# Performance work log

Measured on AMD Instinct MI355X. Metric: run time of the kernel, lower is better.

Reference implementation:

```python
import jax, jax.numpy as jnp
import numpy as np

EMBED_DIM = 1024
NUM_HEADS = 16
HEAD_DIM = EMBED_DIM // NUM_HEADS
BSZ = 8
SEQ = 1024


def setup_inputs() -> dict:
    key = jax.random.key(0)
    ks = jax.random.split(key, 8)
    s = 1.0 / np.sqrt(EMBED_DIM)
    return {
        "query": jax.random.normal(ks[0], (BSZ, SEQ, EMBED_DIM), jnp.float32),
        "key": jax.random.normal(ks[1], (BSZ, SEQ, EMBED_DIM), jnp.float32),
        "value": jax.random.normal(ks[2], (BSZ, SEQ, EMBED_DIM), jnp.float32),
        "Wq": jax.random.normal(ks[3], (EMBED_DIM, EMBED_DIM), jnp.float32) * s,
        "bq": jnp.zeros((EMBED_DIM,), jnp.float32),
        "Wk": jax.random.normal(ks[4], (EMBED_DIM, EMBED_DIM), jnp.float32) * s,
        "bk": jnp.zeros((EMBED_DIM,), jnp.float32),
        "Wv": jax.random.normal(ks[5], (EMBED_DIM, EMBED_DIM), jnp.float32) * s,
        "bv": jnp.zeros((EMBED_DIM,), jnp.float32),
        "Wo": jax.random.normal(ks[6], (EMBED_DIM, EMBED_DIM), jnp.float32) * s,
        "bo": jnp.zeros((EMBED_DIM,), jnp.float32),
    }


def reference(query, key, value, Wq, bq, Wk, bk, Wv, bv, Wo, bo):
    # B=0 path of hfta MultiheadAttention, dropout=0 (eval), no masks.
    bsz, tgt_len, embed_dim = query.shape
    src_len = key.shape[1]
    scaling = HEAD_DIM ** -0.5

    # torch Linear: y = x @ W.T + b
    q = (jnp.einsum('bte,fe->btf', query, Wq) + bq) * scaling
    k = jnp.einsum('bse,fe->bsf', key, Wk) + bk
    v = jnp.einsum('bse,fe->bsf', value, Wv) + bv

    # split heads: [b, h, t, d]
    q = q.reshape(bsz, tgt_len, NUM_HEADS, HEAD_DIM).transpose(0, 2, 1, 3)
    k = k.reshape(bsz, src_len, NUM_HEADS, HEAD_DIM).transpose(0, 2, 1, 3)
    v = v.reshape(bsz, src_len, NUM_HEADS, HEAD_DIM).transpose(0, 2, 1, 3)

    scores = jnp.einsum('bhtd,bhsd->bhts', q, k)          # [b,h,t,s]
    attn = jax.nn.softmax(scores, axis=-1)
    o = jnp.einsum('bhts,bhsd->bhtd', attn, v)            # [b,h,t,d]
    o = o.transpose(0, 2, 1, 3).reshape(bsz, tgt_len, embed_dim)
    o = jnp.einsum('bte,fe->btf', o, Wo) + bo
    return o
```

## Files before the change

### kernel.cpp

```cpp
#include <hip/hip_runtime.h>
#include <hip/hip_bf16.h>

#define BSZ   8
#define SEQ   1024
#define EMB   1024
#define NH    16
#define HD    64
#define MROWS (BSZ*SEQ)
#define LOG2E 1.44269504088896f

typedef short  short8  __attribute__((ext_vector_type(8)));
typedef short  short4v __attribute__((ext_vector_type(4)));
typedef float  floatx4 __attribute__((ext_vector_type(4)));
typedef unsigned int uint2v __attribute__((ext_vector_type(2)));
typedef unsigned int uint4v __attribute__((ext_vector_type(4)));

__device__ __forceinline__ unsigned short f2bf(float f) {
  union { float f; unsigned u; } v; v.f = f;
  unsigned r = v.u + 0x7FFFu + ((v.u >> 16) & 1u);
  return (unsigned short)(r >> 16);
}
__device__ __forceinline__ unsigned pk2bf(float a, float b) {
  __hip_bfloat162 t = __float22bfloat162_rn(make_float2(a, b));
  union { __hip_bfloat162 h; unsigned u; } c; c.h = t; return c.u;
}

__device__ __forceinline__ void g2lds16(const unsigned short* g, unsigned short* l) {
  __builtin_amdgcn_global_load_lds(
      (const __attribute__((address_space(1))) unsigned int*)g,
      (__attribute__((address_space(3))) unsigned int*)l, 16, 0, 0);
}

__global__ __launch_bounds__(256) void convert_w4(
    const float* __restrict__ w0, const float* __restrict__ w1,
    const float* __restrict__ w2, const float* __restrict__ w3,
    unsigned short* __restrict__ out, float qs)
{
  const int z = blockIdx.y;
  const float* w = (z == 0) ? w0 : (z == 1) ? w1 : (z == 2) ? w2 : w3;
  const float s = (z == 0) ? qs : 1.0f;
  int i = blockIdx.x * 256 + threadIdx.x;
  float4 f = ((const float4*)w)[i];
  short4v p;
  p.x = (short)f2bf(f.x * s); p.y = (short)f2bf(f.y * s);
  p.z = (short)f2bf(f.z * s); p.w = (short)f2bf(f.w * s);
  ((short4v*)(out + (size_t)z * EMB * EMB))[i] = p;
}

template<int QKV>
__global__ __launch_bounds__(256) void gemm_k(
    const float* __restrict__ A0, const float* __restrict__ A1,
    const float* __restrict__ A2,
    const unsigned short* __restrict__ Abf,
    const unsigned short* __restrict__ Wbase,
    const float* __restrict__ b0, const float* __restrict__ b1,
    const float* __restrict__ b2, float qs,
    unsigned short* __restrict__ obf, float* __restrict__ of32)
{
  __shared__ __align__(16) unsigned short As[128 * 64];
  __shared__ __align__(16) unsigned short Ws[128 * 64];
  const int tid  = threadIdx.x;
  const int lane = tid & 63, wid = tid >> 6;
  const int z    = QKV ? blockIdx.z : 0;
  const int n0   = blockIdx.x * 128;
  const int m0   = blockIdx.y * 128;
  const int wm = (wid & 1) * 64, wn = (wid >> 1) * 64;
  const int quad = lane >> 4, ln = lane & 15, e3 = ln & 7;
  const int lrow = lane >> 3;
  const int lcol8 = ((lane & 7) ^ lrow) * 8;

  const unsigned short* W = Wbase + (size_t)z * EMB * EMB;
  const float* Af = QKV ? ((z == 0) ? A0 : (z == 1) ? A1 : A2) : (const float*)0;
  const int ar = tid >> 1;
  const int ac = (tid & 1) * 32;

  floatx4 acc[4][4] = {};

  for (int k0 = 0; k0 < EMB; k0 += 64) {
    if (QKV) {
      const float* src = Af + (size_t)(m0 + ar) * EMB + k0 + ac;
#pragma unroll
      for (int i = 0; i < 4; i++) {
        float4 x = *(const float4*)(src + i * 8);
        float4 y = *(const float4*)(src + i * 8 + 4);
        uint4v u;
        u.x = pk2bf(x.x, x.y); u.y = pk2bf(x.z, x.w);
        u.z = pk2bf(y.x, y.y); u.w = pk2bf(y.z, y.w);
        int ch = (4 * (tid & 1) + i) ^ (ar & 7);
        *(uint4v*)&As[ar * 64 + ch * 8] = u;
      }
#pragma unroll
      for (int c = 0; c < 4; c++) {
        int r = wid * 32 + c * 8;
        g2lds16(W + (size_t)(n0 + r + lrow) * EMB + k0 + lcol8, &Ws[r * 64]);
      }
    } else {
#pragma unroll
      for (int c = 0; c < 4; c++) {
        int r = wid * 32 + c * 8;
        g2lds16(Abf + (size_t)(m0 + r + lrow) * EMB + k0 + lcol8, &As[r * 64]);
        g2lds16(W   + (size_t)(n0 + r + lrow) * EMB + k0 + lcol8, &Ws[r * 64]);
      }
    }
    __syncthreads();
#pragma unroll
    for (int ks = 0; ks < 2; ks++) {
      short8 af[4], wf[4];
#pragma unroll
      for (int t = 0; t < 4; t++) {
        int pc = ((4 * ks + quad) ^ e3) * 8;
        af[t] = *(const short8*)&As[(wm + t * 16 + ln) * 64 + pc];
        wf[t] = *(const short8*)&Ws[(wn + t * 16 + ln) * 64 + pc];
      }
#pragma unroll
      for (int mi = 0; mi < 4; mi++)
#pragma unroll
        for (int ni = 0; ni < 4; ni++)
          acc[mi][ni] = __builtin_amdgcn_mfma_f32_16x16x32_bf16(
              af[mi], wf[ni], acc[mi][ni], 0, 0, 0);
    }
    __syncthreads();
  }

  const float* bias = QKV ? ((z == 0) ? b0 : (z == 1) ? b1 : b2) : b0;
  const float bsc = (QKV && z == 0) ? qs : 1.0f;
  unsigned short* outz = obf + (size_t)z * MROWS * EMB;

#pragma unroll
  for (int mi = 0; mi < 4; mi++) {
#pragma unroll
    for (int ni = 0; ni < 4; ni++) {
      int gn = n0 + wn + ni * 16 + ln;
      float bv = bsc * bias[gn];
      int gmb = m0 + wm + mi * 16 + quad * 4;
      if (!QKV) {
#pragma unroll
        for (int r = 0; r < 4; r++)
          of32[(size_t)(gmb + r) * EMB + gn] = acc[mi][ni][r] + bv;
      } else if (z < 2) {
        int h = gn >> 6, d = gn & 63;
#pragma unroll
        for (int r = 0; r < 4; r++) {
          int gm = gmb + r;
          int b = gm >> 10, s = gm & 1023;
          outz[((size_t)(b * NH + h) * SEQ + s) * HD + d] = f2bf(acc[mi][ni][r] + bv);
        }
      } else {
        int h = gn >> 6, d = gn & 63;
        int b = gmb >> 10, s = gmb & 1023;
        short4v pkt;
        pkt.x = (short)f2bf(acc[mi][ni][0] + bv);
        pkt.y = (short)f2bf(acc[mi][ni][1] + bv);
        pkt.z = (short)f2bf(acc[mi][ni][2] + bv);
        pkt.w = (short)f2bf(acc[mi][ni][3] + bv);
        *(short4v*)&outz[((size_t)(b * NH + h) * HD + d) * SEQ + s] = pkt;
      }
    }
  }
}

__global__ __launch_bounds__(256) void attn_k(
    const unsigned short* __restrict__ q,
    const unsigned short* __restrict__ k,
    const unsigned short* __restrict__ vt,
    unsigned short* __restrict__ o)
{
  __shared__ __align__(16) unsigned short Ks[64 * 64];
  __shared__ __align__(16) unsigned short Vs[64 * 64];
  __shared__ __align__(16) unsigned short Pb[4][16][72];
  const int tid  = threadIdx.x;
  const int lane = tid & 63, wv = tid >> 6;
  const int quad = lane >> 4, ln = lane & 15, e3 = ln & 7;
  const int bh = blockIdx.x >> 4;
  const int t0 = (blockIdx.x & 15) * 64 + wv * 16;
  const int b = bh >> 4, h = bh & 15;
  const int lrow = lane >> 3;
  const int lcol8 = ((lane & 7) ^ lrow) * 8;

  const unsigned short* qh = q  + (size_t)bh * SEQ * HD;
  const unsigned short* kh = k  + (size_t)bh * SEQ * HD;
  const unsigned short* vh = vt + (size_t)bh * HD * SEQ;

  short8 qf[2];
#pragma unroll
  for (int kc = 0; kc < 2; kc++)
    qf[kc] = *(const short8*)(qh + (size_t)(t0 + ln) * HD + kc * 32 + quad * 8);

  const short ONE = (short)0x3F80;
  const short8 onesf = {ONE, ONE, ONE, ONE, ONE, ONE, ONE, ONE};

  floatx4 Oa[4] = {};
  floatx4 Ol  = {};

  for (int s0 = 0; s0 < SEQ; s0 += 64) {
#pragma unroll
    for (int c = 0; c < 2; c++) {
      int ch = wv * 2 + c;
      g2lds16(kh + (size_t)(s0 + ch * 8 + lrow) * HD + lcol8,  &Ks[ch * 8 * 64]);
      g2lds16(vh + (size_t)(ch * 8 + lrow) * SEQ + s0 + lcol8, &Vs[ch * 8 * 64]);
    }
    __syncthreads();

    floatx4 sc[4];
#pragma unroll
    for (int st = 0; st < 4; st++) {
      floatx4 a = {};
      short8 kf0 = *(const short8*)&Ks[(st * 16 + ln) * 64 + ((0 + quad) ^ e3) * 8];
      short8 kf1 = *(const short8*)&Ks[(st * 16 + ln) * 64 + ((4 + quad) ^ e3) * 8];
      a = __builtin_amdgcn_mfma_f32_16x16x32_bf16(kf0, qf[0], a, 0, 0, 0);
      a = __builtin_amdgcn_mfma_f32_16x16x32_bf16(kf1, qf[1], a, 0, 0, 0);
      sc[st] = a;
    }

#pragma unroll
    for (int st = 0; st < 4; st++) {
      uint2v u;
      u.x = pk2bf(exp2f(sc[st][0]), exp2f(sc[st][1]));
      u.y = pk2bf(exp2f(sc[st][2]), exp2f(sc[st][3]));
      *(uint2v*)&Pb[wv][ln][st * 16 + quad * 4] = u;
    }

#pragma unroll
    for (int kc = 0; kc < 2; kc++) {
      short8 pf = *(const short8*)&Pb[wv][ln][kc * 32 + quad * 8];
#pragma unroll
      for (int di = 0; di < 4; di++) {
        short8 vf = *(const short8*)&Vs[(di * 16 + ln) * 64 + ((4 * kc + quad) ^ e3) * 8];
        Oa[di] = __builtin_amdgcn_mfma_f32_16x16x32_bf16(vf, pf, Oa[di], 0, 0, 0);
      }
      Ol = __builtin_amdgcn_mfma_f32_16x16x32_bf16(onesf, pf, Ol, 0, 0, 0);
    }
    __syncthreads();
  }

  float linv = 1.0f / Ol[0];
  size_t rowbase = (size_t)(b * SEQ + t0 + ln) * EMB + h * HD;
#pragma unroll
  for (int di = 0; di < 4; di++) {
    uint2v pkt;
    pkt.x = pk2bf(Oa[di][0] * linv, Oa[di][1] * linv);
    pkt.y = pk2bf(Oa[di][2] * linv, Oa[di][3] * linv);
    *(uint2v*)&o[rowbase + di * 16 + quad * 4] = pkt;
  }
}

extern "C" void kernel_launch(void* const* d_in, const int* in_sizes, int n_in,
                              void* d_out, int out_size, void* d_ws, size_t ws_size,
                              hipStream_t stream) {
  const float* query = (const float*)d_in[0];
  const float* key   = (const float*)d_in[1];
  const float* value = (const float*)d_in[2];
  const float* Wq = (const float*)d_in[3];
  const float* bq = (const float*)d_in[4];
  const float* Wk = (const float*)d_in[5];
  const float* bk = (const float*)d_in[6];
  const float* Wv = (const float*)d_in[7];
  const float* bv = (const float*)d_in[8];
  const float* Wo = (const float*)d_in[9];
  const float* bo = (const float*)d_in[10];
  float* out = (float*)d_out;

  unsigned short* ws = (unsigned short*)d_ws;
  const size_t WSZ = (size_t)EMB * EMB;
  const size_t TSZ = (size_t)MROWS * EMB;
  unsigned short* Wb   = ws;
  unsigned short* q_b  = Wb + 4 * WSZ;
  unsigned short* k_b  = q_b + TSZ;
  unsigned short* vt_b = k_b + TSZ;
  unsigned short* o_b  = vt_b + TSZ;

  const float qscale = 0.125f * LOG2E;

  convert_w4<<<dim3((int)(WSZ / 4 / 256), 4), 256, 0, stream>>>(Wq, Wk, Wv, Wo, Wb, qscale);

  gemm_k<1><<<dim3(EMB / 128, MROWS / 128, 3), 256, 0, stream>>>(
      query, key, value, (const unsigned short*)0, Wb,
      bq, bk, bv, qscale, q_b, (float*)0);

  attn_k<<<dim3(BSZ * NH * (SEQ / 64)), 256, 0, stream>>>(q_b, k_b, vt_b, o_b);

  gemm_k<0><<<dim3(EMB / 128, MROWS / 128, 1), 256, 0, stream>>>(
      (const float*)0, (const float*)0, (const float*)0, o_b, Wb + 3 * WSZ,
      bo, (const float*)0, (const float*)0, 1.0f, (unsigned short*)0, out);
}
```

Baseline: 385.3 us.

## Double-buffer GEMM and attention LDS tiles; process four query tiles per attention block

```diff
diff --git a/kernel.cpp b/kernel.cpp
--- a/kernel.cpp
+++ b/kernel.cpp
@@ -48,7 +48,7 @@
 }
 
 template<int QKV>
-__global__ __launch_bounds__(256) void gemm_k(
+__global__ __launch_bounds__(256, 2) void gemm_k(
     const float* __restrict__ A0, const float* __restrict__ A1,
     const float* __restrict__ A2,
     const unsigned short* __restrict__ Abf,
@@ -57,8 +57,8 @@
     const float* __restrict__ b2, float qs,
     unsigned short* __restrict__ obf, float* __restrict__ of32)
 {
-  __shared__ __align__(16) unsigned short As[128 * 64];
-  __shared__ __align__(16) unsigned short Ws[128 * 64];
+  __shared__ __align__(16) unsigned short As[2][128 * 64];
+  __shared__ __align__(16) unsigned short Ws[2][128 * 64];
   const int tid  = threadIdx.x;
   const int lane = tid & 63, wid = tid >> 6;
   const int z    = QKV ? blockIdx.z : 0;
@@ -75,42 +75,56 @@
   const int ac = (tid & 1) * 32;
 
   floatx4 acc[4][4] = {};
-
-  for (int k0 = 0; k0 < EMB; k0 += 64) {
-    if (QKV) {
-      const float* src = Af + (size_t)(m0 + ar) * EMB + k0 + ac;
-#pragma unroll
-      for (int i = 0; i < 4; i++) {
-        float4 x = *(const float4*)(src + i * 8);
-        float4 y = *(const float4*)(src + i * 8 + 4);
-        uint4v u;
-        u.x = pk2bf(x.x, x.y); u.y = pk2bf(x.z, x.w);
-        u.z = pk2bf(y.x, y.y); u.w = pk2bf(y.z, y.w);
-        int ch = (4 * (tid & 1) + i) ^ (ar & 7);
-        *(uint4v*)&As[ar * 64 + ch * 8] = u;
+  float4 ax[8];
+
+  if (QKV) {
+    const float* src = Af + (size_t)(m0 + ar) * EMB + ac;
+#pragma unroll
+    for (int i = 0; i < 8; i++) ax[i] = *(const float4*)(src + i * 4);
+  }
+#pragma unroll
+  for (int c = 0; c < 4; c++) {
+    int r = wid * 32 + c * 8;
+    g2lds16(W + (size_t)(n0 + r + lrow) * EMB + lcol8, &Ws[0][r * 64]);
+    if (!QKV) g2lds16(Abf + (size_t)(m0 + r + lrow) * EMB + lcol8, &As[0][r * 64]);
+  }
+  if (QKV) {
+#pragma unroll
+    for (int i = 0; i < 4; i++) {
+      uint4v u;
+      u.x = pk2bf(ax[2*i].x, ax[2*i].y);     u.y = pk2bf(ax[2*i].z, ax[2*i].w);
+      u.z = pk2bf(ax[2*i+1].x, ax[2*i+1].y); u.w = pk2bf(ax[2*i+1].z, ax[2*i+1].w);
+      int ch = (4 * (tid & 1) + i) ^ (ar & 7);
+      *(uint4v*)&As[0][ar * 64 + ch * 8] = u;
+    }
+  }
+
+  const int NK = EMB / 64;
+  for (int it = 0; it < NK; ++it) {
+    __syncthreads();
+    const int cb = it & 1, nb = (it + 1) & 1;
+    if (it < NK - 1) {
+      const int k1 = (it + 1) * 64;
+      if (QKV) {
+        const float* src = Af + (size_t)(m0 + ar) * EMB + k1 + ac;
+#pragma unroll
+        for (int i = 0; i < 8; i++) ax[i] = *(const float4*)(src + i * 4);
       }
 #pragma unroll
       for (int c = 0; c < 4; c++) {
         int r = wid * 32 + c * 8;
-        g2lds16(W + (size_t)(n0 + r + lrow) * EMB + k0 + lcol8, &Ws[r * 64]);
-      }
-    } else {
-#pragma unroll
-      for (int c = 0; c < 4; c++) {
-        int r = wid * 32 + c * 8;
-        g2lds16(Abf + (size_t)(m0 + r + lrow) * EMB + k0 + lcol8, &As[r * 64]);
-        g2lds16(W   + (size_t)(n0 + r + lrow) * EMB + k0 + lcol8, &Ws[r * 64]);
-      }
-    }
-    __syncthreads();
+        g2lds16(W + (size_t)(n0 + r + lrow) * EMB + k1 + lcol8, &Ws[nb][r * 64]);
+        if (!QKV) g2lds16(Abf + (size_t)(m0 + r + lrow) * EMB + k1 + lcol8, &As[nb][r * 64]);
+      }
+    }
 #pragma unroll
     for (int ks = 0; ks < 2; ks++) {
       short8 af[4], wf[4];
 #pragma unroll
       for (int t = 0; t < 4; t++) {
         int pc = ((4 * ks + quad) ^ e3) * 8;
-        af[t] = *(const short8*)&As[(wm + t * 16 + ln) * 64 + pc];
-        wf[t] = *(const short8*)&Ws[(wn + t * 16 + ln) * 64 + pc];
+        af[t] = *(const short8*)&As[cb][(wm + t * 16 + ln) * 64 + pc];
+        wf[t] = *(const short8*)&Ws[cb][(wn + t * 16 + ln) * 64 + pc];
       }
 #pragma unroll
       for (int mi = 0; mi < 4; mi++)
@@ -119,7 +133,16 @@
           acc[mi][ni] = __builtin_amdgcn_mfma_f32_16x16x32_bf16(
               af[mi], wf[ni], acc[mi][ni], 0, 0, 0);
     }
-    __syncthreads();
+    if (QKV && it < NK - 1) {
+#pragma unroll
+      for (int i = 0; i < 4; i++) {
+        uint4v u;
+        u.x = pk2bf(ax[2*i].x, ax[2*i].y);     u.y = pk2bf(ax[2*i].z, ax[2*i].w);
+        u.z = pk2bf(ax[2*i+1].x, ax[2*i+1].y); u.w = pk2bf(ax[2*i+1].z, ax[2*i+1].w);
+        int ch = (4 * (tid & 1) + i) ^ (ar & 7);
+        *(uint4v*)&As[nb][ar * 64 + ch * 8] = u;
+      }
+    }
   }
 
   const float* bias = QKV ? ((z == 0) ? b0 : (z == 1) ? b1 : b2) : b0;
@@ -159,20 +182,20 @@
   }
 }
 
-__global__ __launch_bounds__(256) void attn_k(
+__global__ __launch_bounds__(256, 2) void attn_k(
     const unsigned short* __restrict__ q,
     const unsigned short* __restrict__ k,
     const unsigned short* __restrict__ vt,
     unsigned short* __restrict__ o)
 {
-  __shared__ __align__(16) unsigned short Ks[64 * 64];
-  __shared__ __align__(16) unsigned short Vs[64 * 64];
+  __shared__ __align__(16) unsigned short Ks[2][64 * 64];
+  __shared__ __align__(16) unsigned short Vs[2][64 * 64];
   __shared__ __align__(16) unsigned short Pb[4][16][72];
   const int tid  = threadIdx.x;
   const int lane = tid & 63, wv = tid >> 6;
   const int quad = lane >> 4, ln = lane & 15, e3 = ln & 7;
-  const int bh = blockIdx.x >> 4;
-  const int t0 = (blockIdx.x & 15) * 64 + wv * 16;
+  const int bh = blockIdx.x >> 2;
+  const int tb = (blockIdx.x & 3) * 256;
   const int b = bh >> 4, h = bh & 15;
   const int lrow = lane >> 3;
   const int lcol8 = ((lane & 7) ^ lrow) * 8;
@@ -181,66 +204,88 @@
   const unsigned short* kh = k  + (size_t)bh * SEQ * HD;
   const unsigned short* vh = vt + (size_t)bh * HD * SEQ;
 
-  short8 qf[2];
-#pragma unroll
-  for (int kc = 0; kc < 2; kc++)
-    qf[kc] = *(const short8*)(qh + (size_t)(t0 + ln) * HD + kc * 32 + quad * 8);
+  short8 qf[4][2];
+#pragma unroll
+  for (int tt = 0; tt < 4; tt++)
+#pragma unroll
+    for (int kc = 0; kc < 2; kc++)
+      qf[tt][kc] = *(const short8*)(qh +
+          (size_t)(tb + tt * 64 + wv * 16 + ln) * HD + kc * 32 + quad * 8);
 
   const short ONE = (short)0x3F80;
   const short8 onesf = {ONE, ONE, ONE, ONE, ONE, ONE, ONE, ONE};
 
-  floatx4 Oa[4] = {};
-  floatx4 Ol  = {};
-
-  for (int s0 = 0; s0 < SEQ; s0 += 64) {
-#pragma unroll
-    for (int c = 0; c < 2; c++) {
-      int ch = wv * 2 + c;
-      g2lds16(kh + (size_t)(s0 + ch * 8 + lrow) * HD + lcol8,  &Ks[ch * 8 * 64]);
-      g2lds16(vh + (size_t)(ch * 8 + lrow) * SEQ + s0 + lcol8, &Vs[ch * 8 * 64]);
-    }
+  floatx4 Oa[4][4] = {};
+  floatx4 Ol[4]    = {};
+
+#pragma unroll
+  for (int c = 0; c < 2; c++) {
+    int ch = wv * 2 + c;
+    g2lds16(kh + (size_t)(ch * 8 + lrow) * HD + lcol8,  &Ks[0][ch * 8 * 64]);
+    g2lds16(vh + (size_t)(ch * 8 + lrow) * SEQ + lcol8, &Vs[0][ch * 8 * 64]);
+  }
+
+  for (int it = 0; it < SEQ / 64; ++it) {
     __syncthreads();
-
-    floatx4 sc[4];
+    const int cb = it & 1, nb = (it + 1) & 1;
+    if (it < SEQ / 64 - 1) {
+      const int s1 = (it + 1) * 64;
+#pragma unroll
+      for (int c = 0; c < 2; c++) {
+        int ch = wv * 2 + c;
+        g2lds16(kh + (size_t)(s1 + ch * 8 + lrow) * HD + lcol8,  &Ks[nb][ch * 8 * 64]);
+        g2lds16(vh + (size_t)(ch * 8 + lrow) * SEQ + s1 + lcol8, &Vs[nb][ch * 8 * 64]);
+      }
+    }
+
+    short8 kf[4][2], vf[4][2];
 #pragma unroll
     for (int st = 0; st < 4; st++) {
-      floatx4 a = {};
-      short8 kf0 = *(const short8*)&Ks[(st * 16 + ln) * 64 + ((0 + quad) ^ e3) * 8];
-      short8 kf1 = *(const short8*)&Ks[(st * 16 + ln) * 64 + ((4 + quad) ^ e3) * 8];
-      a = __builtin_amdgcn_mfma_f32_16x16x32_bf16(kf0, qf[0], a, 0, 0, 0);
-      a = __builtin_amdgcn_mfma_f32_16x16x32_bf16(kf1, qf[1], a, 0, 0, 0);
-      sc[st] = a;
-    }
-
-#pragma unroll
-    for (int st = 0; st < 4; st++) {
-      uint2v u;
-      u.x = pk2bf(exp2f(sc[st][0]), exp2f(sc[st][1]));
-      u.y = pk2bf(exp2f(sc[st][2]), exp2f(sc[st][3]));
-      *(uint2v*)&Pb[wv][ln][st * 16 + quad * 4] = u;
-    }
-
-#pragma unroll
-    for (int kc = 0; kc < 2; kc++) {
-      short8 pf = *(const short8*)&Pb[wv][ln][kc * 32 + quad * 8];
-#pragma unroll
-      for (int di = 0; di < 4; di++) {
-        short8 vf = *(const short8*)&Vs[(di * 16 + ln) * 64 + ((4 * kc + quad) ^ e3) * 8];
-        Oa[di] = __builtin_amdgcn_mfma_f32_16x16x32_bf16(vf, pf, Oa[di], 0, 0, 0);
-      }
-      Ol = __builtin_amdgcn_mfma_f32_16x16x32_bf16(onesf, pf, Ol, 0, 0, 0);
-    }
-    __syncthreads();
-  }
-
-  float linv = 1.0f / Ol[0];
-  size_t rowbase = (size_t)(b * SEQ + t0 + ln) * EMB + h * HD;
-#pragma unroll
-  for (int di = 0; di < 4; di++) {
-    uint2v pkt;
-    pkt.x = pk2bf(Oa[di][0] * linv, Oa[di][1] * linv);
-    pkt.y = pk2bf(Oa[di][2] * linv, Oa[di][3] * linv);
-    *(uint2v*)&o[rowbase + di * 16 + quad * 4] = pkt;
+      kf[st][0] = *(const short8*)&Ks[cb][(st * 16 + ln) * 64 + ((0 + quad) ^ e3) * 8];
+      kf[st][1] = *(const short8*)&Ks[cb][(st * 16 + ln) * 64 + ((4 + quad) ^ e3) * 8];
+      vf[st][0] = *(const short8*)&Vs[cb][(st * 16 + ln) * 64 + ((0 + quad) ^ e3) * 8];
+      vf[st][1] = *(const short8*)&Vs[cb][(st * 16 + ln) * 64 + ((4 + quad) ^ e3) * 8];
+    }
+
+#pragma unroll
+    for (int tt = 0; tt < 4; tt++) {
+      floatx4 sc[4];
+#pragma unroll
+      for (int st = 0; st < 4; st++) {
+        floatx4 a = {};
+        a = __builtin_amdgcn_mfma_f32_16x16x32_bf16(kf[st][0], qf[tt][0], a, 0, 0, 0);
+        a = __builtin_amdgcn_mfma_f32_16x16x32_bf16(kf[st][1], qf[tt][1], a, 0, 0, 0);
+        sc[st] = a;
+      }
+#pragma unroll
+      for (int st = 0; st < 4; st++) {
+        uint2v u;
+        u.x = pk2bf(exp2f(sc[st][0]), exp2f(sc[st][1]));
+        u.y = pk2bf(exp2f(sc[st][2]), exp2f(sc[st][3]));
+        *(uint2v*)&Pb[wv][ln][st * 16 + quad * 4] = u;
+      }
+#pragma unroll
+      for (int kc = 0; kc < 2; kc++) {
+        short8 pf = *(const short8*)&Pb[wv][ln][kc * 32 + quad * 8];
+#pragma unroll
+        for (int di = 0; di < 4; di++)
+          Oa[tt][di] = __builtin_amdgcn_mfma_f32_16x16x32_bf16(vf[di][kc], pf, Oa[tt][di], 0, 0, 0);
+        Ol[tt] = __builtin_amdgcn_mfma_f32_16x16x32_bf16(onesf, pf, Ol[tt], 0, 0, 0);
+      }
+    }
+  }
+
+#pragma unroll
+  for (int tt = 0; tt < 4; tt++) {
+    float linv = 1.0f / Ol[tt][0];
+    size_t rowbase = (size_t)(b * SEQ + tb + tt * 64 + wv * 16 + ln) * EMB + h * HD;
+#pragma unroll
+    for (int di = 0; di < 4; di++) {
+      uint2v pkt;
+      pkt.x = pk2bf(Oa[tt][di][0] * linv, Oa[tt][di][1] * linv);
+      pkt.y = pk2bf(Oa[tt][di][2] * linv, Oa[tt][di][3] * linv);
+      *(uint2v*)&o[rowbase + di * 16 + quad * 4] = pkt;
+    }
   }
 }
 
@@ -277,7 +322,7 @@
       query, key, value, (const unsigned short*)0, Wb,
       bq, bk, bv, qscale, q_b, (float*)0);
 
-  attn_k<<<dim3(BSZ * NH * (SEQ / 64)), 256, 0, stream>>>(q_b, k_b, vt_b, o_b);
+  attn_k<<<dim3(BSZ * NH * (SEQ / 256)), 256, 0, stream>>>(q_b, k_b, vt_b, o_b);
 
   gemm_k<0><<<dim3(EMB / 128, MROWS / 128, 1), 256, 0, stream>>>(
       (const float*)0, (const float*)0, (const float*)0, o_b, Wb + 3 * WSZ,
```

New measurement: 388.8 us. Within noise of the previous version (+0.9%).
